# Optimization experiments

Measured on AMD Instinct MI355X. Metric: run time of the kernel, lower is better.

Reference implementation:

```python
import jax, jax.numpy as jnp
import numpy as np

N = 4096      # num_nodes (unbatched seq len for the transformer)
D = 128       # input_dim = window = d_model
H = 4         # num_heads
DH = D // H
DFF = 2048    # PyTorch TransformerEncoderLayer default dim_feedforward
HID = 256     # hidden_dim
OUT = 64      # output_dim
E = 131072    # num_edges (avg degree 32)
EPS = 1e-5    # LayerNorm eps (torch default)


def layer_norm(x, g, b):
    mu = jnp.mean(x, axis=-1, keepdims=True)
    var = jnp.var(x, axis=-1, keepdims=True)
    return (x - mu) * jax.lax.rsqrt(var + EPS) * g + b


def gcn_conv(x, W, b, src, dst):
    # PyG GCNConv: h = x W^T; add self-loops; symmetric deg^-1/2 norm; scatter-add at dst; + bias
    h = x @ W.T
    loop = jnp.arange(N)
    s = jnp.concatenate([src, loop])
    t = jnp.concatenate([dst, loop])
    deg = jax.ops.segment_sum(jnp.ones_like(t, dtype=h.dtype), t, num_segments=N)
    dinv = jnp.where(deg > 0, jax.lax.rsqrt(jnp.maximum(deg, 1e-12)), 0.0)
    norm = dinv[s] * dinv[t]                                   # [E+N]
    out = jax.ops.segment_sum(h[s] * norm[:, None], t, num_segments=N)
    return out + b


def setup_inputs() -> dict:
    key = jax.random.key(0)
    ks = jax.random.split(key, 12)
    sc = 0.05
    w = lambda k, shape: jax.random.normal(k, shape, dtype=jnp.float32) * sc
    return {
        "x": jax.random.normal(ks[0], (N, D), dtype=jnp.float32),
        "edge_index": jax.random.randint(ks[1], (2, E), 0, N),
        "in_proj_w": w(ks[2], (3 * D, D)),
        "in_proj_b": jnp.zeros((3 * D,), jnp.float32),
        "out_proj_w": w(ks[3], (D, D)),
        "out_proj_b": jnp.zeros((D,), jnp.float32),
        "ln1_g": jnp.ones((D,), jnp.float32),
        "ln1_b": jnp.zeros((D,), jnp.float32),
        "ffn_w1": w(ks[4], (DFF, D)),
        "ffn_b1": jnp.zeros((DFF,), jnp.float32),
        "ffn_w2": w(ks[5], (D, DFF)),
        "ffn_b2": jnp.zeros((D,), jnp.float32),
        "ln2_g": jnp.ones((D,), jnp.float32),
        "ln2_b": jnp.zeros((D,), jnp.float32),
        "gcn1_w": w(ks[6], (HID, D)),
        "gcn1_b": jnp.zeros((HID,), jnp.float32),
        "gcn2_w": w(ks[7], (HID, HID)),
        "gcn2_b": jnp.zeros((HID,), jnp.float32),
        "gcn3_w": w(ks[8], (OUT, HID)),
        "gcn3_b": jnp.zeros((OUT,), jnp.float32),
    }


def reference(x, edge_index, in_proj_w, in_proj_b, out_proj_w, out_proj_b,
              ln1_g, ln1_b, ffn_w1, ffn_b1, ffn_w2, ffn_b2, ln2_g, ln2_b,
              gcn1_w, gcn1_b, gcn2_w, gcn2_b, gcn3_w, gcn3_b):
    src, dst = edge_index[0], edge_index[1]
    # --- TransformerEncoderLayer (post-norm, relu, dropout=0, unbatched [N, D]) ---
    qkv = x @ in_proj_w.T + in_proj_b
    q, k, v = jnp.split(qkv, 3, axis=-1)
    q = q.reshape(N, H, DH)
    k = k.reshape(N, H, DH)
    v = v.reshape(N, H, DH)
    scores = jnp.einsum('nhd,mhd->hnm', q, k) / jnp.sqrt(jnp.float32(DH))
    attn = jax.nn.softmax(scores, axis=-1)
    ctx = jnp.einsum('hnm,mhd->nhd', attn, v).reshape(N, D)
    attn_out = ctx @ out_proj_w.T + out_proj_b
    y = layer_norm(x + attn_out, ln1_g, ln1_b)
    ff = jax.nn.relu(y @ ffn_w1.T + ffn_b1) @ ffn_w2.T + ffn_b2
    z = layer_norm(y + ff, ln2_g, ln2_b)
    # x.squeeze(-1) is a no-op since window (=128) > 1
    # --- 3-layer GCN with ReLU between layers ---
    h = jax.nn.relu(gcn_conv(z, gcn1_w, gcn1_b, src, dst))
    h = jax.nn.relu(gcn_conv(h, gcn2_w, gcn2_b, src, dst))
    return gcn_conv(h, gcn3_w, gcn3_b, src, dst)
```

## Files before the change

### kernel.cpp

```cpp
#include <hip/hip_runtime.h>


typedef unsigned short u16;
typedef __attribute__((ext_vector_type(8))) short bf16x8;
typedef __attribute__((ext_vector_type(4))) float f32x4;

__device__ __forceinline__ float b2f(u16 u) {
  union { unsigned int i; float f; } x; x.i = ((unsigned int)u) << 16; return x.f;
}
__device__ __forceinline__ u16 f2b(float f) {
  union { float f; unsigned int i; } x; x.f = f;
  unsigned int r = x.i + 0x7FFFu + ((x.i >> 16) & 1u);
  return (u16)(r >> 16);
}
__device__ __forceinline__ float ld1(const void* p, size_t i, int bf) {
  return bf ? b2f(((const u16*)p)[i]) : ((const float*)p)[i];
}

__device__ void gemm_body(
    int bx, int by, int bz, int nz,
    const void* __restrict__ A, const void* __restrict__ B,
    const void* __restrict__ bias, void* __restrict__ C, void* __restrict__ C2,
    int N, int K, int lda, int ldb, int bRow0, int bK0, int flags,
    const int* __restrict__ dflag, const float* __restrict__ divL)
{
  const int wbf = *dflag;
  const int abf = (flags & 64) ? 0 : ((flags & 16) ? wbf : 1);
  __shared__ u16 As[64][128];
  __shared__ u16 Bs[64][128];
  const int tid = threadIdx.x;
  const int wv = tid >> 6, l = tid & 63;
  const int lr = l & 15, lq = l >> 4;
  const int row0 = by * 64, col0 = bx * 64;
  const int qr = 32 * (wv >> 1), qc = 32 * (wv & 1);
  const int sr = tid >> 2, sb = tid & 3;
  const int Kz = K / nz;
  const int k0 = bz * Kz;
  f32x4 acc[2][2] = {};
  for (int kt = k0; kt < k0 + Kz; kt += 128) {
    __syncthreads();
#pragma unroll
    for (int g = 0; g < 4; g++) {
      int b = sb + 4 * g;
      int cc = b * 8;
      int bs = (b ^ (sr & 15)) * 8;
      size_t offA = (size_t)(row0 + sr) * lda + kt + cc;
      if (abf) {
        *(bf16x8*)&As[sr][bs] = *(const bf16x8*)((const u16*)A + offA);
      } else {
        const float* pf = (const float*)A + offA;
        float iv = divL
            ? 1.0f / divL[(size_t)((kt + cc) >> 5) * 4096 + row0 + sr]
            : 1.0f;
        float4 f0 = *(const float4*)pf, f1 = *(const float4*)(pf + 4);
        u16 t[8] = {f2b(f0.x*iv), f2b(f0.y*iv), f2b(f0.z*iv), f2b(f0.w*iv),
                    f2b(f1.x*iv), f2b(f1.y*iv), f2b(f1.z*iv), f2b(f1.w*iv)};
        *(bf16x8*)&As[sr][bs] = *(bf16x8*)t;
      }
      size_t offB = (size_t)(bRow0 + col0 + sr) * ldb + bK0 + kt + cc;
      if (wbf) {
        *(bf16x8*)&Bs[sr][bs] = *(const bf16x8*)((const u16*)B + offB);
      } else {
        const float* pf = (const float*)B + offB;
        float4 f0 = *(const float4*)pf, f1 = *(const float4*)(pf + 4);
        u16 t[8] = {f2b(f0.x), f2b(f0.y), f2b(f0.z), f2b(f0.w),
                    f2b(f1.x), f2b(f1.y), f2b(f1.z), f2b(f1.w)};
        *(bf16x8*)&Bs[sr][bs] = *(bf16x8*)t;
      }
    }
    __syncthreads();
#pragma unroll
    for (int kk = 0; kk < 4; kk++) {
      int bxs = ((4 * kk + lq) ^ lr) * 8;
      bf16x8 a0 = *(const bf16x8*)&As[qr + lr][bxs];
      bf16x8 a1 = *(const bf16x8*)&As[qr + 16 + lr][bxs];
      bf16x8 b0 = *(const bf16x8*)&Bs[qc + lr][bxs];
      bf16x8 b1 = *(const bf16x8*)&Bs[qc + 16 + lr][bxs];
      acc[0][0] = __builtin_amdgcn_mfma_f32_16x16x32_bf16(a0, b0, acc[0][0], 0, 0, 0);
      acc[0][1] = __builtin_amdgcn_mfma_f32_16x16x32_bf16(a0, b1, acc[0][1], 0, 0, 0);
      acc[1][0] = __builtin_amdgcn_mfma_f32_16x16x32_bf16(a1, b0, acc[1][0], 0, 0, 0);
      acc[1][1] = __builtin_amdgcn_mfma_f32_16x16x32_bf16(a1, b1, acc[1][1], 0, 0, 0);
    }
  }
  if ((flags & 128) && col0 >= 256) {
#pragma unroll
    for (int i = 0; i < 2; i++) {
#pragma unroll
      for (int j = 0; j < 2; j++) {
        int colg = col0 + qc + 16 * j + lr;
        int d = colg - 256;
        int rowbase = row0 + qr + 16 * i + lq * 4;
        float bb = ld1(bias, colg, wbf);
        ushort4 pv = make_ushort4(
            f2b(acc[i][j][0] + bb), f2b(acc[i][j][1] + bb),
            f2b(acc[i][j][2] + bb), f2b(acc[i][j][3] + bb));
        *(ushort4*)((u16*)C2 + (size_t)d * 4096 + rowbase) = pv;
      }
    }
    return;
  }
  const int ldc = (flags & 128) ? 256 : N;
#pragma unroll
  for (int i = 0; i < 2; i++) {
#pragma unroll
    for (int j = 0; j < 2; j++) {
#pragma unroll
      for (int r = 0; r < 4; r++) {
        int row = row0 + qr + 16 * i + lq * 4 + r;
        int col = col0 + qc + 16 * j + lr;
        float v = acc[i][j][r];
        if (flags & 8) v += ld1(bias, bRow0 + col, wbf);
        if (flags & 1) v = fmaxf(v, 0.f);
        size_t idx = (size_t)row * ldc + col;
        if (flags & 32) {
          ((float*)C)[(size_t)bz * 524288 + idx] = v;
        } else if (flags & 4) {
          float* Cf = (float*)C;
          if (flags & 2) v += Cf[idx];
          Cf[idx] = v;
        } else {
          ((u16*)C)[idx] = f2b(v);
        }
      }
    }
  }
}

__global__ __launch_bounds__(256) void gemm_mfma(
    const void* __restrict__ A, const void* __restrict__ B,
    const void* __restrict__ bias, void* __restrict__ C, void* __restrict__ C2,
    int N, int K, int lda, int ldb, int bRow0, int bK0, int flags,
    const int* __restrict__ dflag, const float* __restrict__ divL)
{
  gemm_body(blockIdx.x, blockIdx.y, blockIdx.z, gridDim.z,
            A, B, bias, C, C2, N, K, lda, ldb, bRow0, bK0, flags, dflag, divL);
}

__global__ __launch_bounds__(256) void det_zero(
    const void* __restrict__ x, int* __restrict__ flag,
    int* __restrict__ cursor)
{
  if (blockIdx.x == 0) {
    __shared__ int cnt;
    if (threadIdx.x == 0) cnt = 0;
    __syncthreads();
    const u16* p = (const u16*)x;
    int c = 0;
    for (int i = threadIdx.x; i < 4096; i += 256) {
      int e = (p[i] >> 7) & 0xFF;
      if (e >= 140) c++;
    }
    atomicAdd(&cnt, c);
    __syncthreads();
    if (threadIdx.x == 0) flag[0] = (cnt < 64) ? 1 : 0;
  } else {
    cursor[(blockIdx.x - 1) * 256 + threadIdx.x] = 0;
  }
}

__global__ __launch_bounds__(256) void csr_inproj(
    const void* __restrict__ xin, const void* __restrict__ W,
    const void* __restrict__ bias, void* __restrict__ qkQK, void* __restrict__ Vg,
    const int* __restrict__ dflag,
    const int* __restrict__ src, const int* __restrict__ dst,
    int* __restrict__ cursor, int* __restrict__ csr, int E)
{
  if (blockIdx.x < 384) {
    gemm_body(blockIdx.x % 6, blockIdx.x / 6, 0, 1,
              xin, W, bias, qkQK, Vg, 384, 128, 128, 128, 0, 0,
               8 | 16 | 128, dflag, nullptr);
  } else {
    int e = (blockIdx.x - 384) * 256 + threadIdx.x;
    if (e < E) {
      int t = dst[e];
      int pos = atomicAdd(&cursor[t], 1);
      if (pos < 128) csr[(t << 7) + pos] = src[e];
    }
  }
}

__global__ __launch_bounds__(256) void attn_part(
    const u16* __restrict__ qk, const u16* __restrict__ Vg,
    float* __restrict__ O, float* __restrict__ L)
{
  const int qt = blockIdx.x, h = blockIdx.y, kc = blockIdx.z;
  const int n0 = qt * 64;
  __shared__ u16 Qs[64][32];
  __shared__ u16 Ks[128][32];
  __shared__ u16 Vt[32][128];
  __shared__ u16 Ps[64][128];
  const int tid = threadIdx.x;
  const int wv = tid >> 6, l = tid & 63;
  const int lr = l & 15, lq = l >> 4;
  const int sr = tid >> 2, sb = tid & 3;
  const int kr = tid >> 1, kb = tid & 1;
  const int vr = tid >> 3, vb = tid & 7;
  *(bf16x8*)&Qs[sr][(sb ^ (sr & 3)) * 8] =
      *(const bf16x8*)(qk + (size_t)(n0 + sr) * 256 + h * 32 + sb * 8);
  __syncthreads();
  const float sc = 0.17677669529663687f;
  bf16x8 qf;
  {
    bf16x8 qraw = *(const bf16x8*)&Qs[16 * wv + lr][(lq ^ (lr & 3)) * 8];
#pragma unroll
    for (int t = 0; t < 8; t++)
      qf[t] = (short)f2b(b2f((u16)qraw[t]) * sc);
  }
  f32x4 o0 = {}, o1 = {};
  float psum[4] = {0.f, 0.f, 0.f, 0.f};
  for (int t = 0; t < 8; t++) {
    const int m0 = kc * 1024 + t * 128;
    __syncthreads();
#pragma unroll
    for (int cc = 0; cc < 2; cc++) {
      int ch = kb + 2 * cc;
      *(bf16x8*)&Ks[kr][(ch ^ (kr & 3)) * 8] =
          *(const bf16x8*)(qk + (size_t)(m0 + kr) * 256 + 128 + h * 32 + ch * 8);
    }
#pragma unroll
    for (int cc = 0; cc < 2; cc++) {
      int ch = vb + 8 * cc;
      *(bf16x8*)&Vt[vr][(ch ^ (vr & 15)) * 8] =
          *(const bf16x8*)(Vg + (size_t)(h * 32 + vr) * 4096 + m0 + ch * 8);
    }
    __syncthreads();
    f32x4 s[8];
#pragma unroll
    for (int jt = 0; jt < 8; jt++) {
      bf16x8 kf = *(const bf16x8*)&Ks[16 * jt + lr][(lq ^ (lr & 3)) * 8];
      f32x4 z = {};
      s[jt] = __builtin_amdgcn_mfma_f32_16x16x32_bf16(qf, kf, z, 0, 0, 0);
    }
#pragma unroll
    for (int jt = 0; jt < 8; jt++)
#pragma unroll
      for (int r = 0; r < 4; r++) {
        float p = __expf(s[jt][r]);
        psum[r] += p;
        int qrow = 16 * wv + lq * 4 + r;
        int ch = 2 * jt + (lr >> 3);
        Ps[qrow][(ch ^ (qrow & 15)) * 8 + (lr & 7)] = f2b(p);
      }
    __syncthreads();
#pragma unroll
    for (int kk = 0; kk < 4; kk++) {
      int prow = 16 * wv + lr;
      bf16x8 pf = *(const bf16x8*)&Ps[prow][((4 * kk + lq) ^ (lr & 15)) * 8];
      bf16x8 v0 = *(const bf16x8*)&Vt[lr][((4 * kk + lq) ^ (lr & 15)) * 8];
      bf16x8 v1 = *(const bf16x8*)&Vt[16 + lr][((4 * kk + lq) ^ (lr & 15)) * 8];
      o0 = __builtin_amdgcn_mfma_f32_16x16x32_bf16(pf, v0, o0, 0, 0, 0);
      o1 = __builtin_amdgcn_mfma_f32_16x16x32_bf16(pf, v1, o1, 0, 0, 0);
    }
  }
  const size_t ko = (size_t)kc * 524288;
  float* Lk = L + (size_t)kc * 16384;
#pragma unroll
  for (int r = 0; r < 4; r++) {
    int row = n0 + 16 * wv + lq * 4 + r;
    O[ko + (size_t)row * 128 + h * 32 + lr]      = o0[r];
    O[ko + (size_t)row * 128 + h * 32 + 16 + lr] = o1[r];
    float ps = psum[r];
    ps += __shfl_xor(ps, 1); ps += __shfl_xor(ps, 2);
    ps += __shfl_xor(ps, 4); ps += __shfl_xor(ps, 8);
    if (lr == 0) Lk[h * 4096 + row] = ps;
  }
}

__global__ __launch_bounds__(256) void oproj_ln(
    const float* __restrict__ Op, const float* __restrict__ Lp,
    const void* __restrict__ W, const void* __restrict__ bias,
    const void* __restrict__ x, const void* __restrict__ g,
    const void* __restrict__ bln, u16* __restrict__ y_bf,
    float* __restrict__ y_f32, const int* __restrict__ dflag)
{
  const int wbf = *dflag;
  __shared__ u16 As[16][128];
  __shared__ u16 Bs[128][128];
  const int tid = threadIdx.x;
  const int r0 = blockIdx.x * 16;
  {
    int r = tid >> 4, b = tid & 15;
    int hh = b >> 2;
    float Ls = Lp[hh * 4096 + r0 + r] + Lp[16384 + hh * 4096 + r0 + r]
             + Lp[32768 + hh * 4096 + r0 + r] + Lp[49152 + hh * 4096 + r0 + r];
    float iv = 1.0f / Ls;
    float a8[8] = {};
#pragma unroll
    for (int kc = 0; kc < 4; kc++) {
      const float* p = Op + (size_t)kc * 524288 + (size_t)(r0 + r) * 128 + b * 8;
      float4 q0 = *(const float4*)p, q1 = *(const float4*)(p + 4);
      a8[0] += q0.x; a8[1] += q0.y; a8[2] += q0.z; a8[3] += q0.w;
      a8[4] += q1.x; a8[5] += q1.y; a8[6] += q1.z; a8[7] += q1.w;
    }
    u16 t[8];
#pragma unroll
    for (int j = 0; j < 8; j++) t[j] = f2b(a8[j] * iv);
    *(bf16x8*)&As[r][(b ^ r) * 8] = *(bf16x8*)t;
  }
  {
    int o = tid >> 1, half = tid & 1;
#pragma unroll
    for (int bb8 = 0; bb8 < 8; bb8++) {
      int b = half * 8 + bb8;
      size_t off = (size_t)o * 128 + b * 8;
      if (wbf) {
        *(bf16x8*)&Bs[o][(b ^ (o & 15)) * 8] = *(const bf16x8*)((const u16*)W + off);
      } else {
        const float* pf = (const float*)W + off;
        float4 f0 = *(const float4*)pf, f1 = *(const float4*)(pf + 4);
        u16 t[8] = {f2b(f0.x), f2b(f0.y), f2b(f0.z), f2b(f0.w),
                    f2b(f1.x), f2b(f1.y), f2b(f1.z), f2b(f1.w)};
        *(bf16x8*)&Bs[o][(b ^ (o & 15)) * 8] = *(bf16x8*)t;
      }
    }
  }
  __syncthreads();
  const int wv = tid >> 6, l = tid & 63;
  const int lr = l & 15, lq = l >> 4;
  const int c0 = 32 * wv;
  f32x4 acc[2] = {};
#pragma unroll
  for (int kk = 0; kk < 4; kk++) {
    int bxs = ((4 * kk + lq) ^ lr) * 8;
    bf16x8 a0 = *(const bf16x8*)&As[lr][bxs];
    bf16x8 b0 = *(const bf16x8*)&Bs[c0 + lr][bxs];
    bf16x8 b1 = *(const bf16x8*)&Bs[c0 + 16 + lr][bxs];
    acc[0] = __builtin_amdgcn_mfma_f32_16x16x32_bf16(a0, b0, acc[0], 0, 0, 0);
    acc[1] = __builtin_amdgcn_mfma_f32_16x16x32_bf16(a0, b1, acc[1], 0, 0, 0);
  }
  __syncthreads();
  float* Cf = (float*)&Bs[0][0];
#pragma unroll
  for (int j = 0; j < 2; j++)
#pragma unroll
    for (int r = 0; r < 4; r++) {
      int row = lq * 4 + r, col = c0 + 16 * j + lr;
      float v = acc[j][r] + ld1(bias, col, wbf)
              + ld1(x, (size_t)(r0 + row) * 128 + col, wbf);
      Cf[row * 128 + col] = v;
    }
  __syncthreads();
#pragma unroll
  for (int it = 0; it < 4; it++) {
    int row = it * 4 + wv;
    float v0 = Cf[row * 128 + l], v1 = Cf[row * 128 + 64 + l];
    float s = v0 + v1, sq = v0 * v0 + v1 * v1;
    for (int off = 32; off; off >>= 1) { s += __shfl_down(s, off); sq += __shfl_down(sq, off); }
    s = __shfl(s, 0); sq = __shfl(sq, 0);
    float mu = s * (1.f / 128.f);
    float var = sq * (1.f / 128.f) - mu * mu;
    float rs = rsqrtf(var + 1e-5f);
    float o0 = (v0 - mu) * rs * ld1(g, l, wbf) + ld1(bln, l, wbf);
    float o1 = (v1 - mu) * rs * ld1(g, l + 64, wbf) + ld1(bln, l + 64, wbf);
    size_t i0 = (size_t)(r0 + row) * 128 + l;
    y_bf[i0] = f2b(o0); y_bf[i0 + 64] = f2b(o1);
    y_f32[i0] = o0; y_f32[i0 + 64] = o1;
  }
}

__global__ __launch_bounds__(256) void ln_res(
    const void* __restrict__ A, int a_mode, const float* __restrict__ R,
    int nacc, const void* __restrict__ rbias,
    const void* __restrict__ g, const void* __restrict__ b,
    u16* __restrict__ out_bf, float* __restrict__ out_f32,
    const int* __restrict__ dflag)
{
  const int wbf = *dflag;
  const int abf = a_mode ? wbf : 0;
  int row = blockIdx.x * 4 + (threadIdx.x >> 6);
  int lane = threadIdx.x & 63;
  size_t i0 = (size_t)row * 128 + lane, i1 = i0 + 64;
  float r0a = 0.f, r1a = 0.f;
  for (int z = 0; z < nacc; z++) {
    r0a += R[(size_t)z * 524288 + i0];
    r1a += R[(size_t)z * 524288 + i1];
  }
  float v0 = ld1(A, i0, abf) + r0a;
  float v1 = ld1(A, i1, abf) + r1a;
  if (rbias) { v0 += ld1(rbias, lane, wbf); v1 += ld1(rbias, lane + 64, wbf); }
  float s = v0 + v1, sq = v0 * v0 + v1 * v1;
  for (int off = 32; off; off >>= 1) { s += __shfl_down(s, off); sq += __shfl_down(sq, off); }
  s = __shfl(s, 0); sq = __shfl(sq, 0);
  float mu = s * (1.f / 128.f);
  float var = sq * (1.f / 128.f) - mu * mu;
  float rs = rsqrtf(var + 1e-5f);
  float r0 = (v0 - mu) * rs * ld1(g, lane, wbf) + ld1(b, lane, wbf);
  float r1 = (v1 - mu) * rs * ld1(g, lane + 64, wbf) + ld1(b, lane + 64, wbf);
  out_bf[i0] = f2b(r0);
  out_bf[i1] = f2b(r1);
  if (out_f32) { out_f32[i0] = r0; out_f32[i1] = r1; }
}

__global__ __launch_bounds__(256) void gcn_gather8(
    const u16* __restrict__ h, const int* __restrict__ deg,
    const int* __restrict__ csr, u16* __restrict__ out, int F)
{
  const int ft = F >> 3;
  const int tpn = ft << 1;
  const int node = blockIdx.x * (256 / tpn) + threadIdx.x / tpn;
  const int sub = (threadIdx.x % tpn) / ft;
  const int f = (threadIdx.x % ft) * 8;
  const int dn = deg[node];
  float di = rsqrtf((float)(dn + 1));
  float a[8] = {};
  if (sub == 0) {
    bf16x8 hv = *(const bf16x8*)(h + (size_t)node * F + f);
#pragma unroll
    for (int j = 0; j < 8; j++) a[j] = di * b2f((u16)hv[j]);
  }
  int e0 = node << 7, e1 = e0 + dn;
  for (int e = e0 + sub; e < e1; e += 2) {
    int s = csr[e];
    float ds = rsqrtf((float)(deg[s] + 1));
    bf16x8 sv = *(const bf16x8*)(h + (size_t)s * F + f);
#pragma unroll
    for (int j = 0; j < 8; j++) a[j] += ds * b2f((u16)sv[j]);
  }
#pragma unroll
  for (int j = 0; j < 8; j++) a[j] += __shfl_xor(a[j], ft);
  if (sub) return;
  u16 t[8];
#pragma unroll
  for (int j = 0; j < 8; j++) t[j] = f2b(a[j] * di);
  *(bf16x8*)(out + (size_t)node * F + f) = *(bf16x8*)t;
}

__global__ __launch_bounds__(256) void gcn_gather(
    const u16* __restrict__ h, const int* __restrict__ deg,
    const int* __restrict__ csr,
    const void* __restrict__ bias, void* __restrict__ out,
    int F, int relu, int final_out, const int* __restrict__ dflag)
{
  const int wbf = *dflag;
  const int tpn = F >> 2;
  const int node = blockIdx.x * (256 / tpn) + threadIdx.x / tpn;
  const int f = (threadIdx.x % tpn) * 4;
  const int dn = deg[node];
  float di = rsqrtf((float)(dn + 1));
  ushort4 hv = *(const ushort4*)(h + (size_t)node * F + f);
  float a0 = di * b2f(hv.x), a1 = di * b2f(hv.y);
  float a2 = di * b2f(hv.z), a3 = di * b2f(hv.w);
  int e0 = node << 7, e1 = e0 + dn;
  for (int e = e0; e < e1; e++) {
    int s = csr[e];
    float ds = rsqrtf((float)(deg[s] + 1));
    ushort4 sv = *(const ushort4*)(h + (size_t)s * F + f);
    a0 += ds * b2f(sv.x); a1 += ds * b2f(sv.y);
    a2 += ds * b2f(sv.z); a3 += ds * b2f(sv.w);
  }
  float b0 = bias ? ld1(bias, f, wbf)     : 0.f;
  float b1 = bias ? ld1(bias, f + 1, wbf) : 0.f;
  float b2 = bias ? ld1(bias, f + 2, wbf) : 0.f;
  float b3 = bias ? ld1(bias, f + 3, wbf) : 0.f;
  float v0 = a0 * di + b0, v1 = a1 * di + b1;
  float v2 = a2 * di + b2, v3 = a3 * di + b3;
  if (relu) {
    v0 = fmaxf(v0, 0.f); v1 = fmaxf(v1, 0.f);
    v2 = fmaxf(v2, 0.f); v3 = fmaxf(v3, 0.f);
  }
  size_t idx = (size_t)node * F + f;
  if (!final_out || wbf) {
    *(ushort4*)((u16*)out + idx) = make_ushort4(f2b(v0), f2b(v1), f2b(v2), f2b(v3));
  } else {
    *(float4*)((float*)out + idx) = make_float4(v0, v1, v2, v3);
  }
}

extern "C" void kernel_launch(void* const* d_in, const int* in_sizes, int n_in,
                              void* d_out, int out_size, void* d_ws, size_t ws_size,
                              hipStream_t stream)
{
  const void* x          = d_in[0];
  const int*  edge       = (const int*)d_in[1];
  const void* in_proj_w  = d_in[2];
  const void* in_proj_b  = d_in[3];
  const void* out_proj_w = d_in[4];
  const void* out_proj_b = d_in[5];
  const void* ln1_g      = d_in[6];
  const void* ln1_b      = d_in[7];
  const void* ffn_w1     = d_in[8];
  const void* ffn_b1     = d_in[9];
  const void* ffn_w2     = d_in[10];
  const void* ffn_b2     = d_in[11];
  const void* ln2_g      = d_in[12];
  const void* ln2_b      = d_in[13];
  const void* g1w        = d_in[14];
  const void* g1b        = d_in[15];
  const void* g2w        = d_in[16];
  const void* g2b        = d_in[17];
  const void* g3w        = d_in[18];
  const void* g3b        = d_in[19];
  const int E = in_sizes[1] / 2;
  const int* esrc = edge;
  const int* edst = edge + E;

  char* wsb     = (char*)d_ws;
  u16*   qkQK   = (u16*)(wsb + 0);
  u16*   Vg     = (u16*)(wsb + 2097152);
  float* Op     = (float*)(wsb + 3145728);
  float* Lp     = (float*)(wsb + 11534336);
  int*   cursor = (int*)(wsb + 11796480);
  int*   dflag  = (int*)(wsb + 11812864);
  int*   csr    = (int*)(wsb + 11829248);
  float* y_f32  = (float*)(wsb + 13926400);
  u16*   y_bf   = (u16*)(wsb + 16023552);
  u16*   z_bf   = (u16*)(wsb + 17072128);
  u16*   az     = (u16*)(wsb + 18120704);
  u16*   h1     = (u16*)(wsb + 19169280);
  u16*   ah1    = (u16*)(wsb + 21266432);
  u16*   h2     = (u16*)(wsb + 23363584);
  u16*   t3     = (u16*)(wsb + 25460736);
  u16*   ff1    = (u16*)(wsb + 25985024);
  float* ff2p   = (float*)(wsb + 42762240);

  det_zero<<<17, 256, 0, stream>>>(x, dflag, cursor);
  csr_inproj<<<896, 256, 0, stream>>>(x, in_proj_w, in_proj_b, qkQK, Vg, dflag,
      esrc, edst, cursor, csr, E);

  attn_part<<<dim3(64, 4, 4), 256, 0, stream>>>(qkQK, Vg, Op, Lp);
  oproj_ln<<<256, 256, 0, stream>>>(Op, Lp, out_proj_w, out_proj_b, x,
      ln1_g, ln1_b, y_bf, y_f32, dflag);
  gemm_mfma<<<dim3(32, 64), 256, 0, stream>>>(y_bf, ffn_w1, ffn_b1, ff1, nullptr,
      2048, 128, 128, 128, 0, 0,  1 | 8, dflag, nullptr);
  gemm_mfma<<<dim3(2, 64, 8), 256, 0, stream>>>(ff1, ffn_w2, nullptr, ff2p, nullptr,
      128, 2048, 2048, 2048, 0, 0,  32, dflag, nullptr);
  ln_res<<<1024, 256, 0, stream>>>(y_f32, 0, ff2p, 8, ffn_b2, ln2_g, ln2_b,
      z_bf, nullptr, dflag);

  gcn_gather8<<<512, 256, 0, stream>>>(z_bf, cursor, csr, az, 128);
  gemm_mfma<<<dim3(4, 64), 256, 0, stream>>>(az, g1w, g1b, h1, nullptr,
      256, 128, 128, 128, 0, 0,  1 | 8, dflag, nullptr);
  gcn_gather8<<<1024, 256, 0, stream>>>(h1, cursor, csr, ah1, 256);
  gemm_mfma<<<dim3(4, 64), 256, 0, stream>>>(ah1, g2w, g2b, h2, nullptr,
      256, 256, 256, 256, 0, 0,  1 | 8, dflag, nullptr);
  gemm_mfma<<<dim3(1, 64), 256, 0, stream>>>(h2, g3w, nullptr, t3, nullptr,
      64, 256, 256, 256, 0, 0, 0, dflag, nullptr);
  gcn_gather<<<256, 256, 0, stream>>>(t3, cursor, csr, g3b, d_out, 64, 0, 1, dflag);
}
```

Before: 259.1 us.

## Fuse FFN up/down GEMMs with residual LayerNorm; batch CSR index loads in gathers

```diff
diff --git a/kernel.cpp b/kernel.cpp
--- a/kernel.cpp
+++ b/kernel.cpp
@@ -358,37 +358,141 @@
   }
 }
 
-__global__ __launch_bounds__(256) void ln_res(
-    const void* __restrict__ A, int a_mode, const float* __restrict__ R,
-    int nacc, const void* __restrict__ rbias,
-    const void* __restrict__ g, const void* __restrict__ b,
-    u16* __restrict__ out_bf, float* __restrict__ out_f32,
-    const int* __restrict__ dflag)
+__global__ __launch_bounds__(512) void ffn_fused(
+    const u16* __restrict__ y_bf, const float* __restrict__ y_f32,
+    const void* __restrict__ W1, const void* __restrict__ b1,
+    const void* __restrict__ W2, const void* __restrict__ b2,
+    const void* __restrict__ g, const void* __restrict__ bln,
+    u16* __restrict__ z_bf, const int* __restrict__ dflag)
 {
   const int wbf = *dflag;
-  const int abf = a_mode ? wbf : 0;
-  int row = blockIdx.x * 4 + (threadIdx.x >> 6);
-  int lane = threadIdx.x & 63;
-  size_t i0 = (size_t)row * 128 + lane, i1 = i0 + 64;
-  float r0a = 0.f, r1a = 0.f;
-  for (int z = 0; z < nacc; z++) {
-    r0a += R[(size_t)z * 524288 + i0];
-    r1a += R[(size_t)z * 524288 + i1];
-  }
-  float v0 = ld1(A, i0, abf) + r0a;
-  float v1 = ld1(A, i1, abf) + r1a;
-  if (rbias) { v0 += ld1(rbias, lane, wbf); v1 += ld1(rbias, lane + 64, wbf); }
-  float s = v0 + v1, sq = v0 * v0 + v1 * v1;
-  for (int off = 32; off; off >>= 1) { s += __shfl_down(s, off); sq += __shfl_down(sq, off); }
-  s = __shfl(s, 0); sq = __shfl(sq, 0);
-  float mu = s * (1.f / 128.f);
-  float var = sq * (1.f / 128.f) - mu * mu;
-  float rs = rsqrtf(var + 1e-5f);
-  float r0 = (v0 - mu) * rs * ld1(g, lane, wbf) + ld1(b, lane, wbf);
-  float r1 = (v1 - mu) * rs * ld1(g, lane + 64, wbf) + ld1(b, lane + 64, wbf);
-  out_bf[i0] = f2b(r0);
-  out_bf[i1] = f2b(r1);
-  if (out_f32) { out_f32[i0] = r0; out_f32[i1] = r1; }
+  __shared__ u16 W1s[64][128];
+  __shared__ u16 W2s[128][64];
+  __shared__ u16 Ps[32][64];
+  const int tid = threadIdx.x;
+  const int wv = tid >> 6, l = tid & 63;
+  const int lr = l & 15, lq = l >> 4;
+  const int r0 = blockIdx.x * 32;
+  const int m = wv >> 2;
+  const int n = wv & 3;
+
+  bf16x8 ya[4];
+#pragma unroll
+  for (int kk = 0; kk < 4; kk++)
+    ya[kk] = *(const bf16x8*)(y_bf + (size_t)(r0 + m * 16 + lr) * 128 + kk * 32 + lq * 8);
+
+  const int sr1 = tid >> 3, c1 = tid & 7;
+  const int o2  = tid >> 2, c2 = tid & 3;
+  bf16x8 w1b0, w1b1, w2b0, w2b1;
+  float4 w1f[4], w2f[4];
+
+#define FFN_LOAD(c)                                                          \
+  if (wbf) {                                                                 \
+    const u16* p1 = (const u16*)W1 + (size_t)((c) * 64 + sr1) * 128;         \
+    w1b0 = *(const bf16x8*)(p1 + c1 * 8);                                    \
+    w1b1 = *(const bf16x8*)(p1 + (c1 + 8) * 8);                              \
+    const u16* p2 = (const u16*)W2 + (size_t)o2 * 2048 + (c) * 64;           \
+    w2b0 = *(const bf16x8*)(p2 + c2 * 8);                                    \
+    w2b1 = *(const bf16x8*)(p2 + (c2 + 4) * 8);                              \
+  } else {                                                                   \
+    const float* p1 = (const float*)W1 + (size_t)((c) * 64 + sr1) * 128;     \
+    w1f[0] = *(const float4*)(p1 + c1 * 8);                                  \
+    w1f[1] = *(const float4*)(p1 + c1 * 8 + 4);                              \
+    w1f[2] = *(const float4*)(p1 + (c1 + 8) * 8);                            \
+    w1f[3] = *(const float4*)(p1 + (c1 + 8) * 8 + 4);                        \
+    const float* p2 = (const float*)W2 + (size_t)o2 * 2048 + (c) * 64;       \
+    w2f[0] = *(const float4*)(p2 + c2 * 8);                                  \
+    w2f[1] = *(const float4*)(p2 + c2 * 8 + 4);                              \
+    w2f[2] = *(const float4*)(p2 + (c2 + 4) * 8);                            \
+    w2f[3] = *(const float4*)(p2 + (c2 + 4) * 8 + 4);                        \
+  }
+
+  FFN_LOAD(0);
+  f32x4 acc2[2] = {};
+  for (int c = 0; c < 32; c++) {
+    __syncthreads();
+    if (wbf) {
+      *(bf16x8*)&W1s[sr1][(c1 ^ (sr1 & 15)) * 8] = w1b0;
+      *(bf16x8*)&W1s[sr1][((c1 + 8) ^ (sr1 & 15)) * 8] = w1b1;
+      *(bf16x8*)&W2s[o2][(c2 ^ (o2 & 7)) * 8] = w2b0;
+      *(bf16x8*)&W2s[o2][((c2 + 4) ^ (o2 & 7)) * 8] = w2b1;
+    } else {
+      u16 t[8];
+      t[0]=f2b(w1f[0].x); t[1]=f2b(w1f[0].y); t[2]=f2b(w1f[0].z); t[3]=f2b(w1f[0].w);
+      t[4]=f2b(w1f[1].x); t[5]=f2b(w1f[1].y); t[6]=f2b(w1f[1].z); t[7]=f2b(w1f[1].w);
+      *(bf16x8*)&W1s[sr1][(c1 ^ (sr1 & 15)) * 8] = *(bf16x8*)t;
+      t[0]=f2b(w1f[2].x); t[1]=f2b(w1f[2].y); t[2]=f2b(w1f[2].z); t[3]=f2b(w1f[2].w);
+      t[4]=f2b(w1f[3].x); t[5]=f2b(w1f[3].y); t[6]=f2b(w1f[3].z); t[7]=f2b(w1f[3].w);
+      *(bf16x8*)&W1s[sr1][((c1 + 8) ^ (sr1 & 15)) * 8] = *(bf16x8*)t;
+      t[0]=f2b(w2f[0].x); t[1]=f2b(w2f[0].y); t[2]=f2b(w2f[0].z); t[3]=f2b(w2f[0].w);
+      t[4]=f2b(w2f[1].x); t[5]=f2b(w2f[1].y); t[6]=f2b(w2f[1].z); t[7]=f2b(w2f[1].w);
+      *(bf16x8*)&W2s[o2][(c2 ^ (o2 & 7)) * 8] = *(bf16x8*)t;
+      t[0]=f2b(w2f[2].x); t[1]=f2b(w2f[2].y); t[2]=f2b(w2f[2].z); t[3]=f2b(w2f[2].w);
+      t[4]=f2b(w2f[3].x); t[5]=f2b(w2f[3].y); t[6]=f2b(w2f[3].z); t[7]=f2b(w2f[3].w);
+      *(bf16x8*)&W2s[o2][((c2 + 4) ^ (o2 & 7)) * 8] = *(bf16x8*)t;
+    }
+    if (c < 31) { FFN_LOAD(c + 1); }
+    __syncthreads();
+    f32x4 s1 = {};
+#pragma unroll
+    for (int kk = 0; kk < 4; kk++) {
+      bf16x8 bfr = *(const bf16x8*)&W1s[n * 16 + lr][((4 * kk + lq) ^ lr) * 8];
+      s1 = __builtin_amdgcn_mfma_f32_16x16x32_bf16(ya[kk], bfr, s1, 0, 0, 0);
+    }
+    {
+      int col = n * 16 + lr;
+      float bb = ld1(b1, c * 64 + col, wbf);
+      int c8 = col >> 3;
+#pragma unroll
+      for (int r = 0; r < 4; r++) {
+        int row = m * 16 + lq * 4 + r;
+        float v = fmaxf(s1[r] + bb, 0.f);
+        Ps[row][(c8 ^ (row & 7)) * 8 + (lr & 7)] = f2b(v);
+      }
+    }
+    __syncthreads();
+#pragma unroll
+    for (int kk = 0; kk < 2; kk++) {
+      bf16x8 pf = *(const bf16x8*)&Ps[m * 16 + lr][((4 * kk + lq) ^ (lr & 7)) * 8];
+#pragma unroll
+      for (int j = 0; j < 2; j++) {
+        int nt = n + 4 * j;
+        bf16x8 wf = *(const bf16x8*)&W2s[nt * 16 + lr][((4 * kk + lq) ^ (lr & 7)) * 8];
+        acc2[j] = __builtin_amdgcn_mfma_f32_16x16x32_bf16(pf, wf, acc2[j], 0, 0, 0);
+      }
+    }
+  }
+#undef FFN_LOAD
+  __syncthreads();
+  float* Cf = (float*)&W1s[0][0];
+#pragma unroll
+  for (int j = 0; j < 2; j++) {
+    int nt = n + 4 * j;
+#pragma unroll
+    for (int r = 0; r < 4; r++) {
+      int row = m * 16 + lq * 4 + r, col = nt * 16 + lr;
+      float v = acc2[j][r] + ld1(b2, col, wbf)
+              + y_f32[(size_t)(r0 + row) * 128 + col];
+      Cf[row * 128 + col] = v;
+    }
+  }
+  __syncthreads();
+#pragma unroll
+  for (int it = 0; it < 4; it++) {
+    int row = it * 8 + wv;
+    float v0 = Cf[row * 128 + l], v1 = Cf[row * 128 + 64 + l];
+    float s = v0 + v1, sq = v0 * v0 + v1 * v1;
+    for (int off = 32; off; off >>= 1) { s += __shfl_down(s, off); sq += __shfl_down(sq, off); }
+    s = __shfl(s, 0); sq = __shfl(sq, 0);
+    float mu = s * (1.f / 128.f);
+    float var = sq * (1.f / 128.f) - mu * mu;
+    float rs = rsqrtf(var + 1e-5f);
+    float o0 = (v0 - mu) * rs * ld1(g, l, wbf) + ld1(bln, l, wbf);
+    float o1 = (v1 - mu) * rs * ld1(g, l + 64, wbf) + ld1(bln, l + 64, wbf);
+    size_t i0 = (size_t)(r0 + row) * 128 + l;
+    z_bf[i0] = f2b(o0);
+    z_bf[i0 + 64] = f2b(o1);
+  }
 }
 
 __global__ __launch_bounds__(256) void gcn_gather8(
@@ -398,9 +502,12 @@
   const int ft = F >> 3;
   const int tpn = ft << 1;
   const int node = blockIdx.x * (256 / tpn) + threadIdx.x / tpn;
-  const int sub = (threadIdx.x % tpn) / ft;
-  const int f = (threadIdx.x % ft) * 8;
-  const int dn = deg[node];
+  const int wl = threadIdx.x & 63;
+  const int gl = threadIdx.x % tpn;
+  const int sub = gl / ft;
+  const int f = (gl % ft) * 8;
+  const int gbase = wl - gl;
+  int dn = deg[node]; if (dn > 128) dn = 128;
   float di = rsqrtf((float)(dn + 1));
   float a[8] = {};
   if (sub == 0) {
@@ -408,13 +515,24 @@
 #pragma unroll
     for (int j = 0; j < 8; j++) a[j] = di * b2f((u16)hv[j]);
   }
-  int e0 = node << 7, e1 = e0 + dn;
-  for (int e = e0 + sub; e < e1; e += 2) {
-    int s = csr[e];
-    float ds = rsqrtf((float)(deg[s] + 1));
-    bf16x8 sv = *(const bf16x8*)(h + (size_t)s * F + f);
-#pragma unroll
-    for (int j = 0; j < 8; j++) a[j] += ds * b2f((u16)sv[j]);
+  const int e0 = node << 7;
+  for (int base = 0; base < dn; base += tpn) {
+    int lim = dn - base; if (lim > tpn) lim = tpn;
+    int mi = 0;
+    if (gl < lim) mi = csr[e0 + base + gl];
+    float mds = rsqrtf((float)(deg[mi] + 1));
+    int nj = (lim - sub + 1) >> 1;
+    int njmax = (lim + 1) >> 1;
+    for (int jj = 0; jj < njmax; jj++) {
+      int j2 = 2 * jj + sub;
+      int s = __shfl(mi, gbase + j2);
+      float ds = __shfl(mds, gbase + j2);
+      if (jj < nj) {
+        bf16x8 sv = *(const bf16x8*)(h + (size_t)s * F + f);
+#pragma unroll
+        for (int j = 0; j < 8; j++) a[j] += ds * b2f((u16)sv[j]);
+      }
+    }
   }
 #pragma unroll
   for (int j = 0; j < 8; j++) a[j] += __shfl_xor(a[j], ft);
@@ -429,24 +547,33 @@
     const u16* __restrict__ h, const int* __restrict__ deg,
     const int* __restrict__ csr,
     const void* __restrict__ bias, void* __restrict__ out,
-    int F, int relu, int final_out, const int* __restrict__ dflag)
+    int F, const int* __restrict__ dflag)
 {
   const int wbf = *dflag;
   const int tpn = F >> 2;
   const int node = blockIdx.x * (256 / tpn) + threadIdx.x / tpn;
-  const int f = (threadIdx.x % tpn) * 4;
-  const int dn = deg[node];
+  const int wl = threadIdx.x & 63;
+  const int gl = threadIdx.x % tpn;
+  const int f = gl * 4;
+  const int gbase = wl - gl;
+  int dn = deg[node]; if (dn > 128) dn = 128;
   float di = rsqrtf((float)(dn + 1));
   ushort4 hv = *(const ushort4*)(h + (size_t)node * F + f);
   float a0 = di * b2f(hv.x), a1 = di * b2f(hv.y);
   float a2 = di * b2f(hv.z), a3 = di * b2f(hv.w);
-  int e0 = node << 7, e1 = e0 + dn;
-  for (int e = e0; e < e1; e++) {
-    int s = csr[e];
-    float ds = rsqrtf((float)(deg[s] + 1));
-    ushort4 sv = *(const ushort4*)(h + (size_t)s * F + f);
-    a0 += ds * b2f(sv.x); a1 += ds * b2f(sv.y);
-    a2 += ds * b2f(sv.z); a3 += ds * b2f(sv.w);
+  const int e0 = node << 7;
+  for (int base = 0; base < dn; base += tpn) {
+    int lim = dn - base; if (lim > tpn) lim = tpn;
+    int mi = 0;
+    if (gl < lim) mi = csr[e0 + base + gl];
+    float mds = rsqrtf((float)(deg[mi] + 1));
+    for (int j = 0; j < lim; j++) {
+      int s = __shfl(mi, gbase + j);
+      float ds = __shfl(mds, gbase + j);
+      ushort4 sv = *(const ushort4*)(h + (size_t)s * F + f);
+      a0 += ds * b2f(sv.x); a1 += ds * b2f(sv.y);
+      a2 += ds * b2f(sv.z); a3 += ds * b2f(sv.w);
+    }
   }
   float b0 = bias ? ld1(bias, f, wbf)     : 0.f;
   float b1 = bias ? ld1(bias, f + 1, wbf) : 0.f;
@@ -454,12 +581,8 @@
   float b3 = bias ? ld1(bias, f + 3, wbf) : 0.f;
   float v0 = a0 * di + b0, v1 = a1 * di + b1;
   float v2 = a2 * di + b2, v3 = a3 * di + b3;
-  if (relu) {
-    v0 = fmaxf(v0, 0.f); v1 = fmaxf(v1, 0.f);
-    v2 = fmaxf(v2, 0.f); v3 = fmaxf(v3, 0.f);
-  }
   size_t idx = (size_t)node * F + f;
-  if (!final_out || wbf) {
+  if (wbf) {
     *(ushort4*)((u16*)out + idx) = make_ushort4(f2b(v0), f2b(v1), f2b(v2), f2b(v3));
   } else {
     *(float4*)((float*)out + idx) = make_float4(v0, v1, v2, v3);
@@ -510,8 +633,6 @@
   u16*   ah1    = (u16*)(wsb + 21266432);
   u16*   h2     = (u16*)(wsb + 23363584);
   u16*   t3     = (u16*)(wsb + 25460736);
-  u16*   ff1    = (u16*)(wsb + 25985024);
-  float* ff2p   = (float*)(wsb + 42762240);
 
   det_zero<<<17, 256, 0, stream>>>(x, dflag, cursor);
   csr_inproj<<<896, 256, 0, stream>>>(x, in_proj_w, in_proj_b, qkQK, Vg, dflag,
@@ -520,12 +641,8 @@
   attn_part<<<dim3(64, 4, 4), 256, 0, stream>>>(qkQK, Vg, Op, Lp);
   oproj_ln<<<256, 256, 0, stream>>>(Op, Lp, out_proj_w, out_proj_b, x,
       ln1_g, ln1_b, y_bf, y_f32, dflag);
-  gemm_mfma<<<dim3(32, 64), 256, 0, stream>>>(y_bf, ffn_w1, ffn_b1, ff1, nullptr,
-      2048, 128, 128, 128, 0, 0,  1 | 8, dflag, nullptr);
-  gemm_mfma<<<dim3(2, 64, 8), 256, 0, stream>>>(ff1, ffn_w2, nullptr, ff2p, nullptr,
-      128, 2048, 2048, 2048, 0, 0,  32, dflag, nullptr);
-  ln_res<<<1024, 256, 0, stream>>>(y_f32, 0, ff2p, 8, ffn_b2, ln2_g, ln2_b,
-      z_bf, nullptr, dflag);
+  ffn_fused<<<128, 512, 0, stream>>>(y_bf, y_f32, ffn_w1, ffn_b1,
+      ffn_w2, ffn_b2, ln2_g, ln2_b, z_bf, dflag);
 
   gcn_gather8<<<512, 256, 0, stream>>>(z_bf, cursor, csr, az, 128);
   gemm_mfma<<<dim3(4, 64), 256, 0, stream>>>(az, g1w, g1b, h1, nullptr,
@@ -535,5 +652,5 @@
       256, 256, 256, 256, 0, 0,  1 | 8, dflag, nullptr);
   gemm_mfma<<<dim3(1, 64), 256, 0, stream>>>(h2, g3w, nullptr, t3, nullptr,
       64, 256, 256, 256, 0, 0, 0, dflag, nullptr);
-  gcn_gather<<<256, 256, 0, stream>>>(t3, cursor, csr, g3b, d_out, 64, 0, 1, dflag);
-}
+  gcn_gather<<<256, 256, 0, stream>>>(t3, cursor, csr, g3b, d_out, 64, dflag);
+}
```

Result: slower. 269.0 us (+3.8%).
